# Performance work log

Hardware: AMD Instinct MI355X
Metric: run time of the kernel (lower is better)

Reference implementation:

```python
import jax, jax.numpy as jnp
import numpy as np

NEG_SLOPE = 0.01  # LeakyReLU default
STRIDE = 5        # group_length // 4
EPS = 1e-5        # RMSNorm eps


def leaky_relu(x):
    return jnp.where(x >= 0, x, NEG_SLOPE * x)


def rmsnorm(x, w):
    return x * jax.lax.rsqrt(jnp.mean(x * x, axis=-1, keepdims=True) + EPS) * w


def s6(x, fc1_w, fc1_b, fc2_w, fc2_b, fc3_w, fc3_b, A):
    # x: [B, L, D] with D = 2*d_model; A: [D, N]
    delta = jax.nn.softplus(x @ fc1_w.T + fc1_b)        # [B, L, D]
    Bm = x @ fc2_w.T + fc2_b                             # [B, L, N]
    Cm = x @ fc3_w.T + fc3_b                             # [B, L, N]
    dA = jnp.exp(jnp.einsum('bld,dn->bldn', delta, A))   # [B, L, D, N]
    dBx = jnp.einsum('bld,bln,bld->bldn', delta, Bm, x)  # delta * B * x

    def step(h, inp):
        dA_t, dBx_t = inp
        h = dA_t * h + dBx_t
        return h, h

    B_, L, D, N = dA.shape
    h0 = jnp.zeros((B_, D, N), dtype=x.dtype)
    _, hs = jax.lax.scan(step, h0, (jnp.swapaxes(dA, 0, 1), jnp.swapaxes(dBx, 0, 1)))
    hs = jnp.swapaxes(hs, 0, 1)                          # [B, L, D, N]
    return jnp.einsum('bln,bldn->bld', Cm, hs)           # [B, L, D]


def setup_inputs() -> dict:
    key = jax.random.key(0)
    ks = iter(jax.random.split(key, 32))

    def rn(shape, scale=0.02):
        return scale * jax.random.normal(next(ks), shape, dtype=jnp.float32)

    B, band, gl, d, N, L = 256, 189, 20, 128, 128, 34
    di = 2 * d
    return {
        'x': jax.random.normal(next(ks), (B, 1, band), dtype=jnp.float32),
        'conv_w': rn((d, 1, gl)), 'conv_b': rn((d,)),
        'norm_w': jnp.ones((d,), jnp.float32),
        'inp_w': rn((di, d)), 'inp_b': rn((di,)),
        'seqconv_w': rn((L, L, 3)), 'seqconv_b': rn((L,)),
        'convlin_w': rn((di, di)), 'convlin_b': rn((di,)),
        'fc1_w': rn((di, di)), 'fc1_b': rn((di,)),
        'fc2_w': rn((N, di)), 'fc2_b': rn((N,)),
        'fc3_w': rn((N, di)), 'fc3_b': rn((N,)),
        'A': jnp.ones((di, N), jnp.float32) / jnp.sqrt(jnp.float32(N)),
        'D_w': rn((di, d)), 'D_b': rn((di,)),
        'out_w': rn((d, di)), 'out_b': rn((d,)),
        'fnn1_w': rn((64, L * d)), 'fnn1_b': rn((64,)),
        'fnn2_w': rn((32, 64)), 'fnn2_b': rn((32,)),
    }


def reference(x, conv_w, conv_b, norm_w, inp_w, inp_b, seqconv_w, seqconv_b,
              convlin_w, convlin_b, fc1_w, fc1_b, fc2_w, fc2_b, fc3_w, fc3_b,
              A, D_w, D_b, out_w, out_b, fnn1_w, fnn1_b, fnn2_w, fnn2_b):
    # group division: Conv1d(1, d, k=20, stride=5) + LeakyReLU
    g = jax.lax.conv_general_dilated(x, conv_w, (STRIDE,), [(0, 0)],
                                     dimension_numbers=('NCH', 'OIH', 'NCH'))
    g = leaky_relu(g + conv_b[None, :, None])            # [B, d, L]
    h = jnp.swapaxes(g, 1, 2)                            # [B, L, d]
    # Mamba block
    xn = rmsnorm(h, norm_w)
    xp = xn @ inp_w.T + inp_b                            # [B, L, 2d]
    # Conv1d(seq_len, seq_len, k=3, pad=1): seq axis L is the channel dim
    xc = jax.lax.conv_general_dilated(xp, seqconv_w, (1,), [(1, 1)],
                                      dimension_numbers=('NCH', 'OIH', 'NCH'))
    xc = jax.nn.silu(xc + seqconv_b[None, :, None])
    xc = xc @ convlin_w.T + convlin_b                    # [B, L, 2d]
    xs = s6(xc, fc1_w, fc1_b, fc2_w, fc2_b, fc3_w, fc3_b, A)
    y = jax.nn.silu(xs) * jax.nn.silu(xn @ D_w.T + D_b)  # gated
    y = y @ out_w.T + out_b                              # [B, L, d]
    # FNN head
    f = y.reshape(y.shape[0], -1)                        # [B, L*d]
    f = leaky_relu(f @ fnn1_w.T + fnn1_b)
    return f @ fnn2_w.T + fnn2_b                         # [B, 32]
```

## Files before the change

### kernel.cpp

```cpp
#include <hip/hip_runtime.h>
#include <math.h>


#define NB    256
#define LL    34
#define DD    128
#define DI    256
#define NN    128
#define MM    (NB*LL)

using u16 = unsigned short;
typedef __attribute__((ext_vector_type(8))) short short8;
typedef __attribute__((ext_vector_type(4))) float f32x4;

__device__ __forceinline__ float silu_f(float x)  { return x / (1.f + __expf(-x)); }
__device__ __forceinline__ float softplus_f(float x) {
    return fmaxf(x, 0.f) + __logf(1.f + __expf(-fabsf(x)));
}
__device__ __forceinline__ float leaky_f(float x) { return (x >= 0.f) ? x : 0.01f * x; }

__device__ __forceinline__ u16 f2bf(float x) {
    unsigned u = __float_as_uint(x);
    return (u16)((u + 0x7FFF + ((u >> 16) & 1)) >> 16);
}
__device__ __forceinline__ float bf2f(u16 h) {
    return __uint_as_float(((unsigned)h) << 16);
}
__device__ __forceinline__ void f2pair(float v, u16* h, u16* l) {
    u16 hh = f2bf(v);
    *h = hh;
    *l = f2bf(v - bf2f(hh));
}

__global__ __launch_bounds__(256)
void prep_k(const float* __restrict__ inp_w, const float* __restrict__ D_w,
            const float* __restrict__ fc1_w, const float* __restrict__ fc2_w,
            const float* __restrict__ fc3_w, const float* __restrict__ convlin_w,
            const float* __restrict__ out_w,
            const float* __restrict__ inp_b, const float* __restrict__ D_b,
            const float* __restrict__ fc1_b, const float* __restrict__ fc2_b,
            const float* __restrict__ fc3_b,
            const float* __restrict__ W1, const float* __restrict__ A,
            u16* __restrict__ wc1h, u16* __restrict__ wc1l,
            u16* __restrict__ wc3h, u16* __restrict__ wc3l,
            u16* __restrict__ cvh,  u16* __restrict__ cvl,
            u16* __restrict__ owh,  u16* __restrict__ owl,
            float* __restrict__ bias1, float* __restrict__ bias3,
            float* __restrict__ W1T, int* __restrict__ flag)
{
    const int bx  = blockIdx.x;
    const int tid = threadIdx.x;
    __shared__ float tile[64][65];

    if (bx < 1152) {
        int i = bx * 256 + tid;
        if (i < 65536) {
            float v = (i < 32768) ? inp_w[i] : D_w[i - 32768];
            f2pair(v, &wc1h[i], &wc1l[i]);
        } else if (i < 196608) {
            int j = i - 65536;
            float v = (j < 65536) ? fc1_w[j] : (j < 98304 ? fc2_w[j - 65536] : fc3_w[j - 98304]);
            f2pair(v, &wc3h[j], &wc3l[j]);
        } else if (i < 262144) {
            int j = i - 196608;
            f2pair(convlin_w[j], &cvh[j], &cvl[j]);
        } else if (i < 294912) {
            int j = i - 262144;
            f2pair(out_w[j], &owh[j], &owl[j]);
        }
        if (i < 512)  bias1[i] = (i < 256) ? inp_b[i] : D_b[i - 256];
        else if (i < 1024) {
            int j = i - 512;
            bias3[j] = (j < 256) ? fc1_b[j] : (j < 384 ? fc2_b[j - 256] : fc3_b[j - 384]);
        }
    } else if (bx < 1220) {
        const int bt = bx - 1152;
        for (int p = 0; p < 16; p++) {
            int idx = tid + p * 256;
            int r = idx >> 6, c = idx & 63;
            tile[r][c] = W1[(size_t)r * 4352 + bt * 64 + c];
        }
        __syncthreads();
        for (int p = 0; p < 16; p++) {
            int idx = tid + p * 256;
            int cc = idx >> 6, rr = idx & 63;
            W1T[(size_t)(bt * 64 + cc) * 64 + rr] = tile[rr][cc];
        }
    } else {
        __shared__ int s;
        if (tid == 0) s = 1;
        __syncthreads();
        bool ok = true;
        for (int k = 0; k < 128; k++) {
            int idx = tid + k * 256;
            ok &= (A[idx] == A[idx & ~127]);
        }
        if (!ok) s = 0;
        __syncthreads();
        if (tid == 0) *flag = s;
    }
}

__global__ __launch_bounds__(1024, 1)
void mega2_k(const int* __restrict__ flag,
             const float* __restrict__ x,
             const float* __restrict__ cw, const float* __restrict__ cb,
             const float* __restrict__ nw,
             const u16* __restrict__ wc1h, const u16* __restrict__ wc1l,
             const float* __restrict__ bias1,
             const float* __restrict__ scw, const float* __restrict__ scb,
             const u16* __restrict__ cvh, const u16* __restrict__ cvl,
             const float* __restrict__ clb,
             const u16* __restrict__ wc3h, const u16* __restrict__ wc3l,
             const float* __restrict__ bias3,
             const float* __restrict__ A,
             const u16* __restrict__ owh, const u16* __restrict__ owl,
             const float* __restrict__ outb,
             float* __restrict__ buf1,
             float* __restrict__ buf3,
             u16* __restrict__ bcpair,
             u16* __restrict__ xc2h, u16* __restrict__ xc2l,
             float* __restrict__ fout)
{
    const int b    = blockIdx.x;
    const int tid  = threadIdx.x;
    const int wave = tid >> 6;
    const int lane = tid & 63;
    const int l15  = lane & 15;
    const int lq   = lane >> 4;

    __shared__ __align__(16) char smem[144944];
    float (*sx)[264] = (float (*)[264])(smem);
    float (*sw)[112] = (float (*)[112])(smem + 35904);
    u16 (*sXch)[264] = (u16 (*)[264])(smem);
    u16 (*sXcl)[264] = (u16 (*)[264])(smem + 25344);
    u16 (*sBh)[136]  = (u16 (*)[136])(smem);
    u16 (*sBl)[136]  = (u16 (*)[136])(smem + 13056);
    u16 (*sCh)[136]  = (u16 (*)[136])(smem + 26112);
    u16 (*sCl)[136]  = (u16 (*)[136])(smem + 39168);
    u16 (*sGh)[264]  = (u16 (*)[264])(smem);
    u16 (*sGl)[264]  = (u16 (*)[264])(smem + 25344);
    u16 (*sXnh)[136] = (u16 (*)[136])(smem + 52224);
    u16 (*sXnl)[136] = (u16 (*)[136])(smem + 65280);
    u16 (*sX2h)[264] = (u16 (*)[264])(smem + 52224);
    u16 (*sX2l)[264] = (u16 (*)[264])(smem + 77568);
    float (*sM)[49]  = (float (*)[49])(smem + 102912);
    float (*sDG)[260]= (float (*)[260])(smem + 109584);
    __shared__ float wsumP[16];

    const bool uni = (*flag != 0);

    for (int idx = tid; idx < LL * LL * 3; idx += 1024) {
        int lo = idx / 102;
        int rem = idx - lo * 102;
        int li = rem / 3;
        int k  = rem - li * 3;
        sw[li][lo * 3 + k] = scw[idx];
    }

    {
        const int rp = tid >> 7;
        const int c  = tid & 127;
        for (int pass = 0; pass < 5; pass++) {
            const int rr = pass * 8 + rp;
            float g = 0.f, s = 0.f;
            if (rr < LL) {
                const float* xr = x + (size_t)b * 189 + rr * 5;
                g = cb[c];
                #pragma unroll
                for (int k = 0; k < 20; k++) g = fmaf(xr[k], cw[c * 20 + k], g);
                g = leaky_f(g);
                s = g * g;
            }
            #pragma unroll
            for (int m = 32; m >= 1; m >>= 1) s += __shfl_xor(s, m);
            if ((tid & 63) == 0) wsumP[tid >> 6] = s;
            __syncthreads();
            if (rr < LL) {
                float mean = (wsumP[rp * 2] + wsumP[rp * 2 + 1]) * (1.f / 128.f);
                float inv = 1.f / sqrtf(mean + 1e-5f);
                float v = g * inv * nw[c];
                f2pair(v, &sXnh[rr][c], &sXnl[rr][c]);
            }
            __syncthreads();
        }
    }

    {
        const int c0 = wave * 32;
        f32x4 a1[3][2];
        #pragma unroll
        for (int i = 0; i < 3; i++)
            #pragma unroll
            for (int j = 0; j < 2; j++) a1[i][j] = (f32x4){0.f, 0.f, 0.f, 0.f};

        #pragma unroll
        for (int ks = 0; ks < 4; ks++) {
            short8 fh[3], fl[3];
            #pragma unroll
            for (int i = 0; i < 3; i++) {
                fh[i] = *(const short8*)&sXnh[i * 16 + l15][ks * 32 + lq * 8];
                fl[i] = *(const short8*)&sXnl[i * 16 + l15][ks * 32 + lq * 8];
            }
            #pragma unroll
            for (int j = 0; j < 2; j++) {
                const size_t wo = (size_t)(c0 + j * 16 + l15) * 128 + ks * 32 + lq * 8;
                short8 bh = *(const short8*)&wc1h[wo];
                short8 bl = *(const short8*)&wc1l[wo];
                #pragma unroll
                for (int i = 0; i < 3; i++) {
                    a1[i][j] = __builtin_amdgcn_mfma_f32_16x16x32_bf16(fh[i], bh, a1[i][j], 0, 0, 0);
                    a1[i][j] = __builtin_amdgcn_mfma_f32_16x16x32_bf16(fh[i], bl, a1[i][j], 0, 0, 0);
                    a1[i][j] = __builtin_amdgcn_mfma_f32_16x16x32_bf16(fl[i], bh, a1[i][j], 0, 0, 0);
                }
            }
        }
        #pragma unroll
        for (int i = 0; i < 3; i++) {
            int row = i * 16 + lq * 4;
            #pragma unroll
            for (int j = 0; j < 2; j++) {
                int col = c0 + j * 16 + l15;
                float bb = bias1[col];
                #pragma unroll
                for (int r = 0; r < 4; r++) {
                    float v = a1[i][j][r] + bb;
                    int rr = row + r;
                    if (rr < LL) {
                        if (col < 256) {
                            sx[rr][col + 1] = v;
                        } else {
                            sDG[rr][col - 256] = v;
                            if (!uni)
                                buf1[((size_t)b * LL + rr) * 512 + col] = v;
                        }
                    }
                }
            }
        }
    }
    if (tid < LL) { sx[tid][0] = 0.f; sx[tid][257] = 0.f; }
    __syncthreads();

    {
        const int tx  = tid & 63;
        const int ty  = tid >> 6;
        const int j0c = tx * 4;
        const int cbase = (ty < 2) ? ty * 3 : 6 + (ty - 2) * 2;
        const int ccnt  = (ty < 2) ? 3 : 2;

        float cacc[3][4];
        #pragma unroll
        for (int i = 0; i < 3; i++)
            #pragma unroll
            for (int jj = 0; jj < 4; jj++) cacc[i][jj] = 0.f;

        for (int li = 0; li < LL; li++) {
            float4 xa = *(const float4*)&sx[li][j0c];
            float2 xb = *(const float2*)&sx[li][j0c + 4];
            float xv[6] = {xa.x, xa.y, xa.z, xa.w, xb.x, xb.y};
            const float* swr = &sw[li][0];
            #pragma unroll
            for (int i = 0; i < 3; i++) {
                if (i < ccnt) {
                    int lo3 = (cbase + i) * 3;
                    float w0 = swr[lo3 + 0];
                    float w1 = swr[lo3 + 1];
                    float w2 = swr[lo3 + 2];
                    #pragma unroll
                    for (int jj = 0; jj < 4; jj++) {
                        cacc[i][jj] = fmaf(w0, xv[jj],     cacc[i][jj]);
                        cacc[i][jj] = fmaf(w1, xv[jj + 1], cacc[i][jj]);
                        cacc[i][jj] = fmaf(w2, xv[jj + 2], cacc[i][jj]);
                    }
                }
            }
        }
        __syncthreads();

        #pragma unroll
        for (int i = 0; i < 3; i++) {
            if (i < ccnt) {
                int lo = cbase + i;
                float bb = scb[lo];
                ushort4 oh, ol;
                float v0 = silu_f(cacc[i][0] + bb);
                float v1 = silu_f(cacc[i][1] + bb);
                float v2 = silu_f(cacc[i][2] + bb);
                float v3 = silu_f(cacc[i][3] + bb);
                f2pair(v0, &oh.x, &ol.x);
                f2pair(v1, &oh.y, &ol.y);
                f2pair(v2, &oh.z, &ol.z);
                f2pair(v3, &oh.w, &ol.w);
                *(ushort4*)&sXch[lo][j0c] = oh;
                *(ushort4*)&sXcl[lo][j0c] = ol;
            }
        }
    }
    __syncthreads();

    {
        const int c0 = wave * 16;
        f32x4 a2[3];
        #pragma unroll
        for (int i = 0; i < 3; i++) a2[i] = (f32x4){0.f, 0.f, 0.f, 0.f};

        #pragma unroll
        for (int ks = 0; ks < 8; ks++) {
            short8 fh[3], fl[3];
            #pragma unroll
            for (int i = 0; i < 3; i++) {
                fh[i] = *(const short8*)&sXch[i * 16 + l15][ks * 32 + lq * 8];
                fl[i] = *(const short8*)&sXcl[i * 16 + l15][ks * 32 + lq * 8];
            }
            const size_t wo = (size_t)(c0 + l15) * 256 + ks * 32 + lq * 8;
            short8 bh = *(const short8*)&cvh[wo];
            short8 bl = *(const short8*)&cvl[wo];
            #pragma unroll
            for (int i = 0; i < 3; i++) {
                a2[i] = __builtin_amdgcn_mfma_f32_16x16x32_bf16(fh[i], bh, a2[i], 0, 0, 0);
                a2[i] = __builtin_amdgcn_mfma_f32_16x16x32_bf16(fh[i], bl, a2[i], 0, 0, 0);
                a2[i] = __builtin_amdgcn_mfma_f32_16x16x32_bf16(fl[i], bh, a2[i], 0, 0, 0);
            }
        }
        #pragma unroll
        for (int i = 0; i < 3; i++) {
            int row = i * 16 + lq * 4;
            int col = c0 + l15;
            float bb = clb[col];
            #pragma unroll
            for (int r = 0; r < 4; r++) {
                float v = a2[i][r] + bb;
                u16 hh, ll;
                f2pair(v, &hh, &ll);
                sX2h[row + r][col] = hh;
                sX2l[row + r][col] = ll;
                if (!uni && (row + r) < LL) {
                    xc2h[(size_t)(b * LL + row + r) * 256 + col] = hh;
                    xc2l[(size_t)(b * LL + row + r) * 256 + col] = ll;
                }
            }
        }
    }
    __syncthreads();

    {
        const int c0 = wave * 32;
        f32x4 a3[3][2];
        #pragma unroll
        for (int i = 0; i < 3; i++)
            #pragma unroll
            for (int j = 0; j < 2; j++) a3[i][j] = (f32x4){0.f, 0.f, 0.f, 0.f};

        #pragma unroll
        for (int ks = 0; ks < 8; ks++) {
            short8 fh[3], fl[3];
            #pragma unroll
            for (int i = 0; i < 3; i++) {
                fh[i] = *(const short8*)&sX2h[i * 16 + l15][ks * 32 + lq * 8];
                fl[i] = *(const short8*)&sX2l[i * 16 + l15][ks * 32 + lq * 8];
            }
            #pragma unroll
            for (int j = 0; j < 2; j++) {
                const size_t wo = (size_t)(c0 + j * 16 + l15) * 256 + ks * 32 + lq * 8;
                short8 bh = *(const short8*)&wc3h[wo];
                short8 bl = *(const short8*)&wc3l[wo];
                #pragma unroll
                for (int i = 0; i < 3; i++) {
                    a3[i][j] = __builtin_amdgcn_mfma_f32_16x16x32_bf16(fh[i], bh, a3[i][j], 0, 0, 0);
                    a3[i][j] = __builtin_amdgcn_mfma_f32_16x16x32_bf16(fh[i], bl, a3[i][j], 0, 0, 0);
                    a3[i][j] = __builtin_amdgcn_mfma_f32_16x16x32_bf16(fl[i], bh, a3[i][j], 0, 0, 0);
                }
            }
        }
        #pragma unroll
        for (int i = 0; i < 3; i++) {
            int row = i * 16 + lq * 4;
            #pragma unroll
            for (int j = 0; j < 2; j++) {
                int col = c0 + j * 16 + l15;
                float bb = bias3[col];
                #pragma unroll
                for (int r = 0; r < 4; r++) {
                    float v = a3[i][j][r] + bb;
                    int rr = row + r;
                    if (col < 256) {
                        v = softplus_f(v);
                        if (rr < LL) buf3[((size_t)b * LL + rr) * 512 + col] = v;
                    } else {
                        u16 hh, ll;
                        f2pair(v, &hh, &ll);
                        int cc = col & 127;
                        if (col < 384) { sBh[rr][cc] = hh; sBl[rr][cc] = ll; }
                        else           { sCh[rr][cc] = hh; sCl[rr][cc] = ll; }
                        if (!uni && rr < LL) {
                            buf3[((size_t)b * LL + rr) * 512 + col] = v;
                            u16* rb = bcpair + ((size_t)b * LL + rr) * 1024
                                      + ((col < 384) ? 0 : 256) + cc;
                            rb[0]   = hh;
                            rb[128] = ll;
                        }
                    }
                }
            }
        }
    }
    __syncthreads();
    if (!uni) return;

    for (int tt = wave; tt < 9; tt += 16) {
        int ti = tt / 3, tj = tt - ti * 3;
        f32x4 acc = (f32x4){0.f, 0.f, 0.f, 0.f};
        #pragma unroll
        for (int ks = 0; ks < 4; ks++) {
            short8 ch = *(const short8*)&sCh[ti * 16 + l15][ks * 32 + lq * 8];
            short8 cl = *(const short8*)&sCl[ti * 16 + l15][ks * 32 + lq * 8];
            short8 bh = *(const short8*)&sBh[tj * 16 + l15][ks * 32 + lq * 8];
            short8 bl = *(const short8*)&sBl[tj * 16 + l15][ks * 32 + lq * 8];
            acc = __builtin_amdgcn_mfma_f32_16x16x32_bf16(ch, bh, acc, 0, 0, 0);
            acc = __builtin_amdgcn_mfma_f32_16x16x32_bf16(ch, bl, acc, 0, 0, 0);
            acc = __builtin_amdgcn_mfma_f32_16x16x32_bf16(cl, bh, acc, 0, 0, 0);
        }
        #pragma unroll
        for (int r = 0; r < 4; r++) {
            int row = ti * 16 + lq * 4 + r;
            if (row < LL) sM[row][tj * 16 + l15] = acc[r];
        }
    }
    __syncthreads();

    if (tid < 256) {
        const int d = tid;
        const float a_d = A[(size_t)d * NN];
        const float* pDel = buf3 + (size_t)b * LL * 512 + d;

        float u[LL], eS[LL];
        float S = 0.f;
        #pragma unroll
        for (int l = 0; l < LL; l++) {
            float dl = pDel[l * 512];
            S = fmaf(dl, a_d, S);
            eS[l] = __expf(S);
            float xv = bf2f(sX2h[l][d]) + bf2f(sX2l[l][d]);
            u[l] = __expf(-S) * dl * xv;
        }

        #pragma unroll
        for (int l = 0; l < LL; l++) {
            float acc = 0.f;
            for (int t = 0; t <= l; t++) acc = fmaf(sM[l][t], u[t], acc);
            float xs = eS[l] * acc;
            float g = silu_f(xs) * silu_f(sDG[l][d]);
            u16 hh, ll2;
            f2pair(g, &hh, &ll2);
            sGh[l][d] = hh;
            sGl[l][d] = ll2;
        }
    } else {
        u16* zh = &sGh[34][0];
        u16* zl = &sGl[34][0];
        for (int idx = tid - 256; idx < 14 * 264; idx += 768) {
            zh[idx] = 0;
            zl[idx] = 0;
        }
    }
    __syncthreads();

    {
        const int j0 = wave & 7;
        const int i0 = (wave >> 3) ? 2 : 0;
        const int ni = (wave >> 3) ? 1 : 2;
        f32x4 a4[2];
        #pragma unroll
        for (int i = 0; i < 2; i++) a4[i] = (f32x4){0.f, 0.f, 0.f, 0.f};
        #pragma unroll
        for (int ks = 0; ks < 8; ks++) {
            const size_t wo = (size_t)(j0 * 16 + l15) * 256 + ks * 32 + lq * 8;
            short8 bh = *(const short8*)&owh[wo];
            short8 bl = *(const short8*)&owl[wo];
            #pragma unroll
            for (int i = 0; i < 2; i++) {
                if (i < ni) {
                    short8 ah = *(const short8*)&sGh[(i0 + i) * 16 + l15][ks * 32 + lq * 8];
                    short8 al = *(const short8*)&sGl[(i0 + i) * 16 + l15][ks * 32 + lq * 8];
                    a4[i] = __builtin_amdgcn_mfma_f32_16x16x32_bf16(ah, bh, a4[i], 0, 0, 0);
                    a4[i] = __builtin_amdgcn_mfma_f32_16x16x32_bf16(ah, bl, a4[i], 0, 0, 0);
                    a4[i] = __builtin_amdgcn_mfma_f32_16x16x32_bf16(al, bh, a4[i], 0, 0, 0);
                }
            }
        }
        #pragma unroll
        for (int i = 0; i < 2; i++) {
            if (i < ni) {
                int row = (i0 + i) * 16 + lq * 4;
                int col = j0 * 16 + l15;
                float bb = outb[col];
                #pragma unroll
                for (int r = 0; r < 4; r++)
                    if (row + r < LL)
                        fout[(size_t)(b * LL + row + r) * 128 + col] = a4[i][r] + bb;
            }
        }
    }
}

__global__ __launch_bounds__(256)
void scan_fb_k(const int* __restrict__ flag,
               const float* __restrict__ dBC,
               const u16*  __restrict__ Xh, const u16* __restrict__ Xl,
               const float* __restrict__ A,
               const float* __restrict__ DG,
               u16* __restrict__ Gh, u16* __restrict__ Gl)
{
    if (*flag != 0) return;
    const int b  = blockIdx.y;
    const int d0 = blockIdx.x * 64;
    const int tid = threadIdx.x;
    const int sub = tid & 15;
    const int pg  = tid >> 4;
    const int dbase = d0 + pg * 4;
    const int nA = sub * 4;

    float a[4][8], h[4][8];
    #pragma unroll
    for (int dd = 0; dd < 4; dd++) {
        const float* Ar = A + (size_t)(dbase + dd) * NN;
        float4 q0 = *(const float4*)(Ar + nA);
        float4 q1 = *(const float4*)(Ar + 64 + nA);
        a[dd][0]=q0.x; a[dd][1]=q0.y; a[dd][2]=q0.z; a[dd][3]=q0.w;
        a[dd][4]=q1.x; a[dd][5]=q1.y; a[dd][6]=q1.z; a[dd][7]=q1.w;
        #pragma unroll
        for (int j = 0; j < 8; j++) h[dd][j] = 0.f;
    }

    const float* pD  = dBC + (size_t)b * LL * 512 + dbase;
    const float* pBC = dBC + (size_t)b * LL * 512 + 256 + nA;
    const u16*  pXh = Xh  + (size_t)b * LL * 256 + dbase;
    const u16*  pXl = Xl  + (size_t)b * LL * 256 + dbase;
    const float* pG  = DG  + (size_t)b * LL * 512 + 256 + dbase;
    u16* pGh = Gh + (size_t)b * LL * 256 + dbase;
    u16* pGl = Gl + (size_t)b * LL * 256 + dbase;

    for (int l = 0; l < LL; l++) {
        float4  cD  = *(const float4*)(pD);
        ushort4 cXh = *(const ushort4*)(pXh);
        ushort4 cXl = *(const ushort4*)(pXl);
        float4 cB0 = *(const float4*)(pBC);
        float4 cB1 = *(const float4*)(pBC + 64);
        float4 cC0 = *(const float4*)(pBC + 128);
        float4 cC1 = *(const float4*)(pBC + 192);
        pD += 512; pBC += 512; pXh += 256; pXl += 256;

        float xv[4] = { bf2f(cXh.x) + bf2f(cXl.x), bf2f(cXh.y) + bf2f(cXl.y),
                        bf2f(cXh.z) + bf2f(cXl.z), bf2f(cXh.w) + bf2f(cXl.w) };
        float dl[4] = {cD.x, cD.y, cD.z, cD.w};
        float dx[4] = {cD.x * xv[0], cD.y * xv[1], cD.z * xv[2], cD.w * xv[3]};
        float bv[8] = {cB0.x,cB0.y,cB0.z,cB0.w,cB1.x,cB1.y,cB1.z,cB1.w};
        float cv[8] = {cC0.x,cC0.y,cC0.z,cC0.w,cC1.x,cC1.y,cC1.z,cC1.w};

        float accd[4] = {0.f, 0.f, 0.f, 0.f};
        #pragma unroll
        for (int dd = 0; dd < 4; dd++)
            #pragma unroll
            for (int j = 0; j < 8; j++) {
                float dA = __expf(dl[dd] * a[dd][j]);
                h[dd][j] = fmaf(dA, h[dd][j], dx[dd] * bv[j]);
                accd[dd] = fmaf(cv[j], h[dd][j], accd[dd]);
            }
        #pragma unroll
        for (int dd = 0; dd < 4; dd++) {
            float v = accd[dd];
            v += __shfl_xor(v, 1);
            v += __shfl_xor(v, 2);
            v += __shfl_xor(v, 4);
            v += __shfl_xor(v, 8);
            accd[dd] = v;
        }
        if (sub == 0) {
            float4 dg = *(const float4*)(pG);
            ushort4 oh, ol;
            float g0 = silu_f(accd[0]) * silu_f(dg.x);
            float g1 = silu_f(accd[1]) * silu_f(dg.y);
            float g2 = silu_f(accd[2]) * silu_f(dg.z);
            float g3 = silu_f(accd[3]) * silu_f(dg.w);
            f2pair(g0, &oh.x, &ol.x);
            f2pair(g1, &oh.y, &ol.y);
            f2pair(g2, &oh.z, &ol.z);
            f2pair(g3, &oh.w, &ol.w);
            *(ushort4*)pGh = oh;
            *(ushort4*)pGl = ol;
        }
        pG += 512; pGh += 256; pGl += 256;
    }
}

__global__ __launch_bounds__(512)
void tail_cold_k(const int* __restrict__ flag,
                 const u16* __restrict__ gFh, const u16* __restrict__ gFl,
                 const u16* __restrict__ owh, const u16* __restrict__ owl,
                 const float* __restrict__ outb,
                 float* __restrict__ fout)
{
    if (*flag != 0) return;
    const int b    = blockIdx.x;
    const int tid  = threadIdx.x;
    const int wave = tid >> 6;
    const int lane = tid & 63;
    const int l15  = lane & 15;
    const int lq   = lane >> 4;

    __shared__ u16 sGh[48][264];
    __shared__ u16 sGl[48][264];

    for (int idx = tid; idx < LL * 32; idx += 512) {
        int l = idx >> 5, c = (idx & 31) << 3;
        *(short8*)&sGh[l][c] = *(const short8*)&gFh[((size_t)b * LL + l) * 256 + c];
        *(short8*)&sGl[l][c] = *(const short8*)&gFl[((size_t)b * LL + l) * 256 + c];
    }
    {
        u16* zh = &sGh[34][0];
        u16* zl = &sGl[34][0];
        for (int idx = tid; idx < 14 * 264; idx += 512) {
            zh[idx] = 0;
            zl[idx] = 0;
        }
    }
    __syncthreads();

    const int j0 = wave;
    f32x4 a4[3];
    #pragma unroll
    for (int i = 0; i < 3; i++) a4[i] = (f32x4){0.f, 0.f, 0.f, 0.f};
    #pragma unroll
    for (int ks = 0; ks < 8; ks++) {
        const size_t wo = (size_t)(j0 * 16 + l15) * 256 + ks * 32 + lq * 8;
        short8 bh = *(const short8*)&owh[wo];
        short8 bl = *(const short8*)&owl[wo];
        #pragma unroll
        for (int i = 0; i < 3; i++) {
            short8 ah = *(const short8*)&sGh[i * 16 + l15][ks * 32 + lq * 8];
            short8 al = *(const short8*)&sGl[i * 16 + l15][ks * 32 + lq * 8];
            a4[i] = __builtin_amdgcn_mfma_f32_16x16x32_bf16(ah, bh, a4[i], 0, 0, 0);
            a4[i] = __builtin_amdgcn_mfma_f32_16x16x32_bf16(ah, bl, a4[i], 0, 0, 0);
            a4[i] = __builtin_amdgcn_mfma_f32_16x16x32_bf16(al, bh, a4[i], 0, 0, 0);
        }
    }
    #pragma unroll
    for (int i = 0; i < 3; i++) {
        int row = i * 16 + lq * 4;
        int col = j0 * 16 + l15;
        float bb = outb[col];
        #pragma unroll
        for (int r = 0; r < 4; r++)
            if (row + r < LL)
                fout[(size_t)(b * LL + row + r) * 128 + col] = a4[i][r] + bb;
    }
}

__global__ __launch_bounds__(256)
void fnn1_k(const float* __restrict__ F, const float* __restrict__ W1T,
            float* __restrict__ partials)
{
    const int btile = blockIdx.x;
    const int kc    = blockIdx.y;
    const int tid   = threadIdx.x;
    __shared__ float sf[16][260];
    for (int i = tid; i < 16 * 256; i += 256) {
        int r = i >> 8, c = i & 255;
        sf[r][c] = F[(size_t)(btile * 16 + r) * 4352 + kc * 256 + c];
    }
    __syncthreads();

    const int o  = tid & 63;
    const int bq = tid >> 6;
    const float* w = W1T + (size_t)(kc * 256) * 64 + o;
    float acc[4] = {0.f, 0.f, 0.f, 0.f};
    for (int k = 0; k < 256; k += 4) {
        float w0 = w[(size_t)(k + 0) * 64];
        float w1 = w[(size_t)(k + 1) * 64];
        float w2 = w[(size_t)(k + 2) * 64];
        float w3 = w[(size_t)(k + 3) * 64];
        #pragma unroll
        for (int bj = 0; bj < 4; bj++) {
            float4 f4 = *(const float4*)&sf[bq * 4 + bj][k];
            acc[bj] = fmaf(w0, f4.x, acc[bj]);
            acc[bj] = fmaf(w1, f4.y, acc[bj]);
            acc[bj] = fmaf(w2, f4.z, acc[bj]);
            acc[bj] = fmaf(w3, f4.w, acc[bj]);
        }
    }
    #pragma unroll
    for (int bj = 0; bj < 4; bj++)
        partials[(size_t)kc * 16384 + (btile * 16 + bq * 4 + bj) * 64 + o] = acc[bj];
}

__global__ __launch_bounds__(64)
void fnn2_k(const float* __restrict__ partials,
            const float* __restrict__ B1,
            const float* __restrict__ W2, const float* __restrict__ B2,
            float* __restrict__ out)
{
    int b = blockIdx.x;
    int t = threadIdx.x;
    __shared__ float s1[64];
    float acc = B1[t];
    #pragma unroll
    for (int kc = 0; kc < 17; kc++)
        acc += partials[(size_t)kc * 16384 + b * 64 + t];
    s1[t] = leaky_f(acc);
    __syncthreads();

    if (t < 32) {
        float acc2 = B2[t];
        const float* w2 = W2 + t * 64;
        #pragma unroll
        for (int j = 0; j < 64; j++) acc2 = fmaf(s1[j], w2[j], acc2);
        out[(size_t)b * 32 + t] = acc2;
    }
}

extern "C" void kernel_launch(void* const* d_in, const int* in_sizes, int n_in,
                              void* d_out, int out_size, void* d_ws, size_t ws_size,
                              hipStream_t stream)
{
    const float* x        = (const float*)d_in[0];
    const float* conv_w   = (const float*)d_in[1];
    const float* conv_b   = (const float*)d_in[2];
    const float* norm_w   = (const float*)d_in[3];
    const float* inp_w    = (const float*)d_in[4];
    const float* inp_b    = (const float*)d_in[5];
    const float* seqconv_w= (const float*)d_in[6];
    const float* seqconv_b= (const float*)d_in[7];
    const float* convlin_w= (const float*)d_in[8];
    const float* convlin_b= (const float*)d_in[9];
    const float* fc1_w    = (const float*)d_in[10];
    const float* fc1_b    = (const float*)d_in[11];
    const float* fc2_w    = (const float*)d_in[12];
    const float* fc2_b    = (const float*)d_in[13];
    const float* fc3_w    = (const float*)d_in[14];
    const float* fc3_b    = (const float*)d_in[15];
    const float* A        = (const float*)d_in[16];
    const float* D_w      = (const float*)d_in[17];
    const float* D_b      = (const float*)d_in[18];
    const float* out_w    = (const float*)d_in[19];
    const float* out_b    = (const float*)d_in[20];
    const float* fnn1_w   = (const float*)d_in[21];
    const float* fnn1_b   = (const float*)d_in[22];
    const float* fnn2_w   = (const float*)d_in[23];
    const float* fnn2_b   = (const float*)d_in[24];

    char* W = (char*)d_ws;
    float* buf1  = (float*)(W + 0);
    float* buf3  = (float*)(W + 17825792);
    float* fout  = (float*)(W + 35651584);
    u16*   xc2h  = (u16*)  (W + 37879808);
    u16*   xc2l  = (u16*)  (W + 42336256);
    u16*   gateh = (u16*)  (W + 44564480);
    u16*   gatel = (u16*)  (W + 49020928);
    float* w1t   = (float*)(W + 53477376);
    u16*   wc1h  = (u16*)  (W + 54591488);
    u16*   wc1l  = (u16*)  (W + 54722560);
    u16*   wc3h  = (u16*)  (W + 54853632);
    u16*   wc3l  = (u16*)  (W + 55115776);
    u16*   cvh   = (u16*)  (W + 55377920);
    u16*   cvl   = (u16*)  (W + 55508992);
    u16*   owh   = (u16*)  (W + 55640064);
    u16*   owl   = (u16*)  (W + 55705600);
    float* bias1 = (float*)(W + 55771136);
    float* bias3 = (float*)(W + 55773184);
    int*   uflag = (int*)  (W + 55775232);
    u16* bcpair = (u16*)buf1;
    float* partials = buf3;

    prep_k<<<1221, 256, 0, stream>>>(inp_w, D_w, fc1_w, fc2_w, fc3_w,
                                     convlin_w, out_w,
                                     inp_b, D_b, fc1_b, fc2_b, fc3_b,
                                     fnn1_w, A,
                                     wc1h, wc1l, wc3h, wc3l, cvh, cvl,
                                     owh, owl, bias1, bias3, w1t, uflag);

    mega2_k<<<NB, 1024, 0, stream>>>(uflag, x, conv_w, conv_b, norm_w,
                                     wc1h, wc1l, bias1,
                                     seqconv_w, seqconv_b,
                                     cvh, cvl, convlin_b, wc3h, wc3l, bias3,
                                     A, owh, owl, out_b,
                                     buf1, buf3, bcpair, xc2h, xc2l, fout);

    scan_fb_k<<<dim3(4, NB), 256, 0, stream>>>(uflag, buf3, xc2h, xc2l, A,
                                               buf1, gateh, gatel);
    tail_cold_k<<<NB, 512, 0, stream>>>(uflag, gateh, gatel, owh, owl, out_b,
                                        fout);

    fnn1_k<<<dim3(16, 17), 256, 0, stream>>>(fout, w1t, partials);
    fnn2_k<<<NB, 64, 0, stream>>>(partials, fnn1_b, fnn2_w, fnn2_b,
                                  (float*)d_out);
}
```

Before: 204.8 us.

## Per-wave conv+RMSNorm without block barriers and split scan output across all threads

The conv/RMSNorm prologue now gives each wave one sequence row and 128 channels, two per lane. The row sum is reduced with wave shuffles only, which removes the shared-memory partial sums and the two block-wide barriers per pass. The scan-output stage now runs on all 1024 threads. Each group of 256 recomputes the per-channel prefix terms and then handles every fourth time step, and the separate zeroing of the padding rows is dropped. With the time loop no longer unrolled, the u/eS arrays are indexed dynamically and may spill to scratch. The padding rows of the gate buffer are also left uninitialised.

```diff
diff --git a/kernel.cpp b/kernel.cpp
--- a/kernel.cpp
+++ b/kernel.cpp
@@ -146,7 +146,6 @@
     u16 (*sX2l)[264] = (u16 (*)[264])(smem + 77568);
     float (*sM)[49]  = (float (*)[49])(smem + 102912);
     float (*sDG)[260]= (float (*)[260])(smem + 109584);
-    __shared__ float wsumP[16];
 
     const bool uni = (*flag != 0);
 
@@ -157,34 +156,39 @@
         int k  = rem - li * 3;
         sw[li][lo * 3 + k] = scw[idx];
     }
+    if (tid < LL) { sx[tid][0] = 0.f; sx[tid][257] = 0.f; }
 
     {
-        const int rp = tid >> 7;
-        const int c  = tid & 127;
-        for (int pass = 0; pass < 5; pass++) {
-            const int rr = pass * 8 + rp;
-            float g = 0.f, s = 0.f;
+        const int t = lane;
+        #pragma unroll
+        for (int pass = 0; pass < 3; pass++) {
+            const int rr = pass * 16 + wave;
             if (rr < LL) {
                 const float* xr = x + (size_t)b * 189 + rr * 5;
-                g = cb[c];
+                float xv[20];
                 #pragma unroll
-                for (int k = 0; k < 20; k++) g = fmaf(xr[k], cw[c * 20 + k], g);
-                g = leaky_f(g);
-                s = g * g;
-            }
-            #pragma unroll
-            for (int m = 32; m >= 1; m >>= 1) s += __shfl_xor(s, m);
-            if ((tid & 63) == 0) wsumP[tid >> 6] = s;
-            __syncthreads();
-            if (rr < LL) {
-                float mean = (wsumP[rp * 2] + wsumP[rp * 2 + 1]) * (1.f / 128.f);
-                float inv = 1.f / sqrtf(mean + 1e-5f);
-                float v = g * inv * nw[c];
-                f2pair(v, &sXnh[rr][c], &sXnl[rr][c]);
-            }
-            __syncthreads();
-        }
-    }
+                for (int k = 0; k < 20; k++) xv[k] = xr[k];
+                float g0 = cb[t];
+                float g1 = cb[t + 64];
+                #pragma unroll
+                for (int k = 0; k < 20; k++) {
+                    g0 = fmaf(xv[k], cw[t * 20 + k], g0);
+                    g1 = fmaf(xv[k], cw[(t + 64) * 20 + k], g1);
+                }
+                g0 = leaky_f(g0);
+                g1 = leaky_f(g1);
+                float s = fmaf(g1, g1, g0 * g0);
+                #pragma unroll
+                for (int m = 32; m >= 1; m >>= 1) s += __shfl_xor(s, m);
+                float inv = 1.f / sqrtf(s * (1.f / 128.f) + 1e-5f);
+                float v0 = g0 * inv * nw[t];
+                float v1 = g1 * inv * nw[t + 64];
+                f2pair(v0, &sXnh[rr][t], &sXnl[rr][t]);
+                f2pair(v1, &sXnh[rr][t + 64], &sXnl[rr][t + 64]);
+            }
+        }
+    }
+    __syncthreads();
 
     {
         const int c0 = wave * 32;
@@ -239,7 +243,6 @@
             }
         }
     }
-    if (tid < LL) { sx[tid][0] = 0.f; sx[tid][257] = 0.f; }
     __syncthreads();
 
     {
@@ -429,8 +432,9 @@
     }
     __syncthreads();
 
-    if (tid < 256) {
-        const int d = tid;
+    {
+        const int d   = tid & 255;
+        const int grp = tid >> 8;
         const float a_d = A[(size_t)d * NN];
         const float* pDel = buf3 + (size_t)b * LL * 512 + d;
 
@@ -445,8 +449,7 @@
             u[l] = __expf(-S) * dl * xv;
         }
 
-        #pragma unroll
-        for (int l = 0; l < LL; l++) {
+        for (int l = grp; l < LL; l += 4) {
             float acc = 0.f;
             for (int t = 0; t <= l; t++) acc = fmaf(sM[l][t], u[t], acc);
             float xs = eS[l] * acc;
@@ -455,13 +458,6 @@
             f2pair(g, &hh, &ll2);
             sGh[l][d] = hh;
             sGl[l][d] = ll2;
-        }
-    } else {
-        u16* zh = &sGh[34][0];
-        u16* zl = &sGl[34][0];
-        for (int idx = tid - 256; idx < 14 * 264; idx += 768) {
-            zh[idx] = 0;
-            zl[idx] = 0;
         }
     }
     __syncthreads();
```

Measured after the change: 227.7 us. +11.2%, slower.
